# Kernel optimization log

Measured on AMD Instinct MI355X. Metric: run time of the kernel, lower is better.

Reference implementation:

```python
import jax, jax.numpy as jnp
import numpy as np

D_MODEL = 2048
NHEAD = 16
HEAD_DIM = D_MODEL // NHEAD  # 128
B, S = 2, 2048
THETA = 10000.0


def setup_inputs() -> dict:
    key = jax.random.key(0)
    ks = jax.random.split(key, 10)
    sc = 1.0 / np.sqrt(D_MODEL)
    inp = {
        "x": jax.random.normal(ks[0], (B, S, D_MODEL), dtype=jnp.float32),
        "mask": jnp.tril(jnp.ones((1, 1, S, S), dtype=jnp.int32)),
        "Wq": jax.random.normal(ks[1], (D_MODEL, D_MODEL), dtype=jnp.float32) * sc,
        "bq": jax.random.normal(ks[2], (D_MODEL,), dtype=jnp.float32) * 0.01,
        "Wk": jax.random.normal(ks[3], (D_MODEL, D_MODEL), dtype=jnp.float32) * sc,
        "bk": jax.random.normal(ks[4], (D_MODEL,), dtype=jnp.float32) * 0.01,
        "Wv": jax.random.normal(ks[5], (D_MODEL, D_MODEL), dtype=jnp.float32) * sc,
        "bv": jax.random.normal(ks[6], (D_MODEL,), dtype=jnp.float32) * 0.01,
        "Wo": jax.random.normal(ks[7], (D_MODEL, D_MODEL), dtype=jnp.float32) * sc,
        "bo": jax.random.normal(ks[8], (D_MODEL,), dtype=jnp.float32) * 0.01,
    }
    return inp


def _rope(x):
    # x: [B, H, S, D]; rotary applied to first D/2 dims (per the torch module's chunk(2)).
    D = x.shape[-1]
    half = D // 2            # rotary slice size (64)
    quarter = half // 2      # rotate_half split (32)
    seq = x.shape[2]
    inv_freq = 1.0 / (THETA ** (jnp.arange(0, D, 2, dtype=jnp.float32) / D))  # [D/2]
    t = jnp.arange(seq, dtype=jnp.float32)
    freqs = jnp.einsum("i,j->ij", t, inv_freq)  # [S, D/2]
    # emb = cat(freqs, freqs) then sliced to [:half] == freqs[:, :half]
    cos = jnp.cos(freqs)[None, None, :, :half]  # [1,1,S,half]
    sin = jnp.sin(freqs)[None, None, :, :half]
    x_rope, x_pass = x[..., :half], x[..., half:]
    x1, x2 = x_rope[..., :quarter], x_rope[..., quarter:]
    rotated = jnp.concatenate([-x2, x1], axis=-1)
    x_rope = x_rope * cos + rotated * sin
    return jnp.concatenate([x_rope, x_pass], axis=-1)


def reference(x, mask, Wq, bq, Wk, bk, Wv, bv, Wo, bo):
    b, s, _ = x.shape
    def proj(W, bias):
        y = jnp.einsum("bsd,ed->bse", x, W) + bias  # torch Linear: x @ W.T + b
        return y.reshape(b, s, NHEAD, HEAD_DIM).transpose(0, 2, 1, 3)  # [B,H,S,Dh]
    q = _rope(proj(Wq, bq))
    k = _rope(proj(Wk, bk))
    v = proj(Wv, bv)
    scores = jnp.einsum("bhqd,bhkd->bhqk", q, k) / jnp.sqrt(jnp.float32(HEAD_DIM))
    scores = jnp.where(mask == 0, jnp.float32(-1e9), scores)
    a = jax.nn.softmax(scores, axis=-1)
    o = jnp.einsum("bhqk,bhkd->bhqd", a, v)
    o = o.transpose(0, 2, 1, 3).reshape(b, s, D_MODEL)
    return jnp.einsum("bsd,ed->bse", o, Wo) + bo
```

## Files before the change

kernel.cpp:

```cpp
#include <hip/hip_runtime.h>
#include <stdint.h>
#include <math.h>

typedef short short8 __attribute__((ext_vector_type(8)));
typedef float f32x4 __attribute__((ext_vector_type(4)));

#define S_LEN   2048
#define DMODEL  2048
#define NHEADS  16
#define HDIM    128
#define NBATCH  2
#define BHTOT   32
#define MROWS   4096

#define XB_OFF   ((size_t)0)
#define WQ_OFF   ((size_t)16777216)
#define WK_OFF   ((size_t)25165824)
#define WV_OFF   ((size_t)33554432)
#define Q_OFF    ((size_t)41943040)
#define K_OFF    ((size_t)58720256)
#define VT_OFF   ((size_t)75497472)
#define COS_OFF  ((size_t)92274688)
#define SIN_OFF  ((size_t)92798976)
#define WO_OFF   ((size_t)93323264)
#define WS_NEED  (WO_OFF + (size_t)8388608)

__device__ __forceinline__ unsigned short f2bf(float f) {
  unsigned int u = __float_as_uint(f);
  unsigned int r = (u + 0x7FFFu + ((u >> 16) & 1u)) >> 16;
  return (unsigned short)r;
}
__device__ __forceinline__ float bf2f(unsigned short b) {
  return __uint_as_float(((unsigned int)b) << 16);
}

__device__ __forceinline__ void gl_lds16(const unsigned short* g, unsigned short* l) {
  __builtin_amdgcn_global_load_lds(
      (const __attribute__((address_space(1))) unsigned int*)(g),
      (__attribute__((address_space(3))) unsigned int*)(l),
      16, 0, 0);
}

__global__ __launch_bounds__(256) void k_cvt(const float* __restrict__ src,
                                             unsigned short* __restrict__ dst, int n4) {
  int i = blockIdx.x * 256 + threadIdx.x;
  if (i >= n4) return;
  float4 v = ((const float4*)src)[i];
  ushort4 o;
  o.x = f2bf(v.x); o.y = f2bf(v.y); o.z = f2bf(v.z); o.w = f2bf(v.w);
  ((ushort4*)dst)[i] = o;
}

__global__ __launch_bounds__(256) void k_prep(
    const float* __restrict__ x, const float* __restrict__ Wq,
    const float* __restrict__ Wk, const float* __restrict__ Wv,
    const float* __restrict__ Wo,
    unsigned short* __restrict__ xb, unsigned short* __restrict__ wqb,
    unsigned short* __restrict__ wkb, unsigned short* __restrict__ wvb,
    unsigned short* __restrict__ wob,
    float* __restrict__ ct, float* __restrict__ st) {
  int i = blockIdx.x * 256 + threadIdx.x;
  if (i < 6291456) {
    const float* s; unsigned short* d; int off;
    if (i < 2097152) { s = x; d = xb; off = i; }
    else {
      int j = i - 2097152, sel = j >> 20;
      off = j & 1048575;
      if (sel == 3) {
        if (!wob) return;
        s = Wo; d = wob;
      } else {
        s = (sel == 0) ? Wq : (sel == 1 ? Wk : Wv);
        d = (sel == 0) ? wqb : (sel == 1 ? wkb : wvb);
      }
    }
    float4 v = ((const float4*)s)[off];
    ushort4 o;
    o.x = f2bf(v.x); o.y = f2bf(v.y); o.z = f2bf(v.z); o.w = f2bf(v.w);
    ((ushort4*)d)[off] = o;
  } else {
    int j = i - 6291456;
    if (j < S_LEN * 64) {
      int s = j >> 6, jj = j & 63;
      float inv = expf(-(float)(2 * jj) * (9.210340371976184f / 128.0f));
      float ang = (float)s * inv;
      ct[j] = cosf(ang);
      st[j] = sinf(ang);
    }
  }
}

#define CP 136
__global__ __launch_bounds__(256) void k_gemm_qkv(
    const unsigned short* __restrict__ xb,
    const unsigned short* __restrict__ wqb, const unsigned short* __restrict__ wkb,
    const unsigned short* __restrict__ wvb,
    const float* __restrict__ bq, const float* __restrict__ bk, const float* __restrict__ bv,
    const float* __restrict__ ct, const float* __restrict__ st,
    unsigned short* __restrict__ qr, unsigned short* __restrict__ kr,
    unsigned short* __restrict__ vt) {
  __shared__ unsigned short SMEM[128 * CP];
  unsigned short* As = SMEM;
  unsigned short* Bs = SMEM + 8192;
  int m0 = blockIdx.x * 128;
  int n0g = blockIdx.y * 128;
  int wsel = n0g >> 11;
  int nw0 = n0g & (DMODEL - 1);
  const unsigned short* W = (wsel == 0) ? wqb : (wsel == 1 ? wkb : wvb);
  const float* bias = (wsel == 0) ? bq : (wsel == 1 ? bk : bv);
  int tid = threadIdx.x, lane = tid & 63, wid = tid >> 6;
  int wr = wid >> 1, wc = wid & 1;
  int lq = lane & 15, lk = lane >> 4;
  int gr = wid * 32 + (lane >> 3);
  int gc = ((lane & 7) * 8) ^ ((lane >> 3) << 3);

  f32x4 acc[4][4];
#pragma unroll
  for (int m = 0; m < 4; m++)
#pragma unroll
    for (int n = 0; n < 4; n++) { acc[m][n][0]=0.f; acc[m][n][1]=0.f; acc[m][n][2]=0.f; acc[m][n][3]=0.f; }

  for (int k0 = 0; k0 < DMODEL; k0 += 64) {
#pragma unroll
    for (int i = 0; i < 4; i++) {
      gl_lds16(xb + (size_t)(m0 + gr + i * 8) * DMODEL + k0 + gc, As + (wid * 32 + i * 8) * 64);
      gl_lds16(W  + (size_t)(nw0 + gr + i * 8) * DMODEL + k0 + gc, Bs + (wid * 32 + i * 8) * 64);
    }
    __syncthreads();
#pragma unroll
    for (int kk = 0; kk < 2; kk++) {
      short8 af[4], bfr[4];
      int sw = (lq & 7) << 3;
#pragma unroll
      for (int m = 0; m < 4; m++)
        af[m] = *(const short8*)&As[(wr * 64 + m * 16 + lq) * 64 + ((kk * 32 + lk * 8) ^ sw)];
#pragma unroll
      for (int n = 0; n < 4; n++)
        bfr[n] = *(const short8*)&Bs[(wc * 64 + n * 16 + lq) * 64 + ((kk * 32 + lk * 8) ^ sw)];
#pragma unroll
      for (int m = 0; m < 4; m++)
#pragma unroll
        for (int n = 0; n < 4; n++)
          acc[m][n] = __builtin_amdgcn_mfma_f32_16x16x32_bf16(af[m], bfr[n], acc[m][n], 0, 0, 0);
    }
    __syncthreads();
  }

  int h = nw0 >> 7, b = m0 >> 11, s0 = m0 & (S_LEN - 1);
  float bi[4];
#pragma unroll
  for (int n = 0; n < 4; n++) bi[n] = bias[nw0 + wc * 64 + n * 16 + lq];

  if (wsel < 2) {
    float qs = (wsel == 0) ? 0.08838834764831843f : 1.0f;
    if (wc == 0) {
#pragma unroll
      for (int m = 0; m < 4; m++) {
        int sl = wr * 64 + m * 16 + lk * 4;
#pragma unroll
        for (int r = 0; r < 4; r++) {
          int s = (s0 + sl + r);
          const float* cb = ct + s * 64;
          const float* sb = st + s * 64;
#pragma unroll
          for (int n = 0; n < 2; n++) {
            int fq = n * 16 + lq;
            float x1 = acc[m][n][r] + bi[n];
            float x2 = acc[m][n + 2][r] + bi[n + 2];
            SMEM[(sl + r) * CP + fq]      = f2bf((x1 * cb[fq]      - x2 * sb[fq])      * qs);
            SMEM[(sl + r) * CP + fq + 32] = f2bf((x2 * cb[fq + 32] + x1 * sb[fq + 32]) * qs);
          }
        }
      }
    } else {
#pragma unroll
      for (int m = 0; m < 4; m++) {
        int sl = wr * 64 + m * 16 + lk * 4;
#pragma unroll
        for (int n = 0; n < 4; n++) {
          int fq = 64 + n * 16 + lq;
#pragma unroll
          for (int r = 0; r < 4; r++)
            SMEM[(sl + r) * CP + fq] = f2bf((acc[m][n][r] + bi[n]) * qs);
        }
      }
    }
    __syncthreads();
    int row = tid >> 1, hf2 = tid & 1;
    unsigned short* dstb = (wsel == 0 ? qr : kr) +
        ((size_t)(b * NHEADS + h) * S_LEN + s0 + row) * HDIM + hf2 * 64;
    const unsigned short* srcb = &SMEM[row * CP + hf2 * 64];
#pragma unroll
    for (int j = 0; j < 8; j++)
      *(short8*)(dstb + j * 8) = *(const short8*)(srcb + j * 8);
  } else {
#pragma unroll
    for (int m = 0; m < 4; m++) {
      int sl = wr * 64 + m * 16 + lk * 4;
#pragma unroll
      for (int n = 0; n < 4; n++) {
        int fq = wc * 64 + n * 16 + lq;
#pragma unroll
        for (int r = 0; r < 4; r++)
          SMEM[fq * CP + sl + r] = f2bf(acc[m][n][r] + bi[n]);
      }
    }
    __syncthreads();
    int row = tid >> 1, hf2 = tid & 1;
    unsigned short* dstb = vt +
        ((size_t)(b * NHEADS + h) * HDIM + row) * S_LEN + s0 + hf2 * 64;
    const unsigned short* srcb = &SMEM[row * CP + hf2 * 64];
#pragma unroll
    for (int j = 0; j < 8; j++)
      *(short8*)(dstb + j * 8) = *(const short8*)(srcb + j * 8);
  }
}

__device__ __forceinline__ void attn_sm_pv(
    f32x4* sacc, f32x4* acco, float* rm, float* rs,
    unsigned short (*Psw)[72], const unsigned short* V0,
    int lq, int lk, int rsw) {
  float mx4[4];
  int need = 0;
#pragma unroll
  for (int r = 0; r < 4; r++) {
    float mx = fmaxf(fmaxf(sacc[0][r], sacc[1][r]), fmaxf(sacc[2][r], sacc[3][r]));
    mx = fmaxf(mx, __shfl_xor(mx, 1, 64));
    mx = fmaxf(mx, __shfl_xor(mx, 2, 64));
    mx = fmaxf(mx, __shfl_xor(mx, 4, 64));
    mx = fmaxf(mx, __shfl_xor(mx, 8, 64));
    mx4[r] = mx;
    need |= (mx - rm[r] > 8.0f) ? 1 : 0;
  }
  if (__any(need)) {
#pragma unroll
    for (int r = 0; r < 4; r++) {
      float mnew = fmaxf(rm[r], mx4[r]);
      float corr = __expf(rm[r] - mnew);
      rs[r] *= corr;
#pragma unroll
      for (int nd = 0; nd < 8; nd++) acco[nd][r] *= corr;
      rm[r] = mnew;
    }
  }
#pragma unroll
  for (int r = 0; r < 4; r++) {
    float psum = 0.f;
#pragma unroll
    for (int n = 0; n < 4; n++) {
      float p = __expf(sacc[n][r] - rm[r]);
      sacc[n][r] = p;
      psum += p;
    }
    rs[r] += psum;
  }
#pragma unroll
  for (int n = 0; n < 4; n++)
#pragma unroll
    for (int r = 0; r < 4; r++)
      Psw[lk * 4 + r][n * 16 + lq] = f2bf(sacc[n][r]);
#pragma unroll
  for (int ks2 = 0; ks2 < 2; ks2++) {
    short8 pa = *(const short8*)&Psw[lq][ks2 * 32 + lk * 8];
#pragma unroll
    for (int nd = 0; nd < 8; nd++) {
      short8 vf = *(const short8*)&V0[(nd * 16 + lq) * 64 + ((ks2 * 32 + lk * 8) ^ rsw)];
      acco[nd] = __builtin_amdgcn_mfma_f32_16x16x32_bf16(pa, vf, acco[nd], 0, 0, 0);
    }
  }
}

__global__ __launch_bounds__(256, 2) void k_attn(
    const unsigned short* __restrict__ qr, const unsigned short* __restrict__ kr,
    const unsigned short* __restrict__ vt, unsigned short* __restrict__ ob) {
  __shared__ unsigned short Kl[2][64 * 128];
  __shared__ unsigned short Vl[2][128 * 64];
  __shared__ unsigned short Ps[4][16][72];
  int bh = blockIdx.x;
  int yy = blockIdx.y;
  int f = (yy < 8) ? yy : 23 - yy;
  int qtA = 31 - f, qtB = f;
  int q0A = qtA * 64, q0B = qtB * 64;
  int b = bh >> 4, h = bh & 15;
  int tid = threadIdx.x, lane = tid & 63, w = tid >> 6;
  int lq = lane & 15, lk = lane >> 4;
  const unsigned short* kbh = kr + (size_t)bh * S_LEN * HDIM;
  const unsigned short* vbh = vt + (size_t)bh * HDIM * S_LEN;
  int ksrow = tid >> 4;
  int kscol = ((tid & 15) * 8) ^ ((ksrow & 7) << 3);
  int vsrow = tid >> 3;
  int vscol = ((tid & 7) * 8) ^ ((vsrow & 7) << 3);
  int ldso = tid * 8;
  int rsw = (lq & 7) << 3;

  const unsigned short* qbA =
      qr + ((size_t)bh * S_LEN + q0A + w * 16 + lq) * HDIM + lk * 8;
  const unsigned short* qbB =
      qr + ((size_t)bh * S_LEN + q0B + w * 16 + lq) * HDIM + lk * 8;
  short8 qfA[4], qfB[4];
#pragma unroll
  for (int ks = 0; ks < 4; ks++) {
    qfA[ks] = *(const short8*)(qbA + ks * 32);
    qfB[ks] = *(const short8*)(qbB + ks * 32);
  }

  f32x4 accoA[8], accoB[8];
#pragma unroll
  for (int nd = 0; nd < 8; nd++) {
    accoA[nd][0]=0.f; accoA[nd][1]=0.f; accoA[nd][2]=0.f; accoA[nd][3]=0.f;
    accoB[nd][0]=0.f; accoB[nd][1]=0.f; accoB[nd][2]=0.f; accoB[nd][3]=0.f;
  }
  float rmA[4], rsA[4], rmB[4], rsB[4];
#pragma unroll
  for (int r = 0; r < 4; r++) { rmA[r] = -3.0e38f; rsA[r] = 0.f; rmB[r] = -3.0e38f; rsB[r] = 0.f; }

#pragma unroll
  for (int c = 0; c < 4; c++) {
    gl_lds16(kbh + (size_t)(c * 16 + ksrow) * HDIM + kscol, &Kl[0][c * 2048 + ldso]);
    gl_lds16(vbh + (size_t)(c * 32 + vsrow) * S_LEN + vscol, &Vl[0][c * 2048 + ldso]);
  }
  __syncthreads();
  int cur = 0;

  for (int t = 0; t <= qtA; t++) {
    int kv0 = t * 64;
    if (t < qtA) {
      int nx = kv0 + 64;
#pragma unroll
      for (int c = 0; c < 4; c++) {
        gl_lds16(kbh + (size_t)(nx + c * 16 + ksrow) * HDIM + kscol,
                 &Kl[cur ^ 1][c * 2048 + ldso]);
        gl_lds16(vbh + (size_t)(c * 32 + vsrow) * S_LEN + nx + vscol,
                 &Vl[cur ^ 1][c * 2048 + ldso]);
      }
    }
    const unsigned short* K0 = &Kl[cur][0];
    const unsigned short* V0 = &Vl[cur][0];
    bool actB = (t <= qtB);

    f32x4 saccA[4], saccB[4];
#pragma unroll
    for (int n = 0; n < 4; n++) {
      saccA[n][0]=0.f; saccA[n][1]=0.f; saccA[n][2]=0.f; saccA[n][3]=0.f;
      saccB[n][0]=0.f; saccB[n][1]=0.f; saccB[n][2]=0.f; saccB[n][3]=0.f;
    }
    if (actB) {
#pragma unroll
      for (int ks = 0; ks < 4; ks++)
#pragma unroll
        for (int n = 0; n < 4; n++) {
          short8 kf = *(const short8*)&K0[(n * 16 + lq) * 128 + ((ks * 32 + lk * 8) ^ rsw)];
          saccA[n] = __builtin_amdgcn_mfma_f32_16x16x32_bf16(qfA[ks], kf, saccA[n], 0, 0, 0);
          saccB[n] = __builtin_amdgcn_mfma_f32_16x16x32_bf16(qfB[ks], kf, saccB[n], 0, 0, 0);
        }
    } else {
#pragma unroll
      for (int ks = 0; ks < 4; ks++)
#pragma unroll
        for (int n = 0; n < 4; n++) {
          short8 kf = *(const short8*)&K0[(n * 16 + lq) * 128 + ((ks * 32 + lk * 8) ^ rsw)];
          saccA[n] = __builtin_amdgcn_mfma_f32_16x16x32_bf16(qfA[ks], kf, saccA[n], 0, 0, 0);
        }
    }
    if (t == qtA) {
#pragma unroll
      for (int n = 0; n < 4; n++)
#pragma unroll
        for (int r = 0; r < 4; r++) {
          int qrow = q0A + w * 16 + lk * 4 + r;
          int kvc = kv0 + n * 16 + lq;
          if (kvc > qrow) saccA[n][r] = -3.0e38f;
        }
    }
    attn_sm_pv(saccA, accoA, rmA, rsA, Ps[w], V0, lq, lk, rsw);
    if (actB) {
      if (t == qtB) {
#pragma unroll
        for (int n = 0; n < 4; n++)
#pragma unroll
          for (int r = 0; r < 4; r++) {
            int qrow = q0B + w * 16 + lk * 4 + r;
            int kvc = kv0 + n * 16 + lq;
            if (kvc > qrow) saccB[n][r] = -3.0e38f;
          }
      }
      attn_sm_pv(saccB, accoB, rmB, rsB, Ps[w], V0, lq, lk, rsw);
    }
    __syncthreads();
    cur ^= 1;
  }

#pragma unroll
  for (int r = 0; r < 4; r++) {
    float sA = rsA[r];
    sA += __shfl_xor(sA, 1, 64);
    sA += __shfl_xor(sA, 2, 64);
    sA += __shfl_xor(sA, 4, 64);
    sA += __shfl_xor(sA, 8, 64);
    float invA = 1.0f / sA;
    int srowA = q0A + w * 16 + lk * 4 + r;
    unsigned short* dstA = ob + ((size_t)b * S_LEN + srowA) * DMODEL + h * HDIM;
#pragma unroll
    for (int nd = 0; nd < 8; nd++) dstA[nd * 16 + lq] = f2bf(accoA[nd][r] * invA);
    float sB = rsB[r];
    sB += __shfl_xor(sB, 1, 64);
    sB += __shfl_xor(sB, 2, 64);
    sB += __shfl_xor(sB, 4, 64);
    sB += __shfl_xor(sB, 8, 64);
    float invB = 1.0f / sB;
    int srowB = q0B + w * 16 + lk * 4 + r;
    unsigned short* dstB = ob + ((size_t)b * S_LEN + srowB) * DMODEL + h * HDIM;
#pragma unroll
    for (int nd = 0; nd < 8; nd++) dstB[nd * 16 + lq] = f2bf(accoB[nd][r] * invB);
  }
}

__global__ __launch_bounds__(256) void k_gemm_out(
    const unsigned short* __restrict__ ob, const unsigned short* __restrict__ wob,
    const float* __restrict__ bo, float* __restrict__ out) {
  __shared__ unsigned short As[128][64];
  __shared__ unsigned short Bs[128][64];
  int m0 = blockIdx.x * 128, n0 = blockIdx.y * 128;
  int tid = threadIdx.x, lane = tid & 63, wid = tid >> 6;
  int wr = wid >> 1, wc = wid & 1;
  int lq = lane & 15, lk = lane >> 4;
  int gr = wid * 32 + (lane >> 3);
  int gc = ((lane & 7) * 8) ^ ((lane >> 3) << 3);

  f32x4 acc[4][4];
#pragma unroll
  for (int m = 0; m < 4; m++)
#pragma unroll
    for (int n = 0; n < 4; n++) { acc[m][n][0]=0.f; acc[m][n][1]=0.f; acc[m][n][2]=0.f; acc[m][n][3]=0.f; }

  for (int k0 = 0; k0 < DMODEL; k0 += 64) {
#pragma unroll
    for (int i = 0; i < 4; i++) {
      gl_lds16(ob  + (size_t)(m0 + gr + i * 8) * DMODEL + k0 + gc, &As[wid * 32 + i * 8][0]);
      gl_lds16(wob + (size_t)(n0 + gr + i * 8) * DMODEL + k0 + gc, &Bs[wid * 32 + i * 8][0]);
    }
    __syncthreads();
#pragma unroll
    for (int kk = 0; kk < 2; kk++) {
      short8 af[4], bfr[4];
      int sw = (lq & 7) << 3;
#pragma unroll
      for (int m = 0; m < 4; m++)
        af[m] = *(const short8*)&As[wr * 64 + m * 16 + lq][(kk * 32 + lk * 8) ^ sw];
#pragma unroll
      for (int n = 0; n < 4; n++)
        bfr[n] = *(const short8*)&Bs[wc * 64 + n * 16 + lq][(kk * 32 + lk * 8) ^ sw];
#pragma unroll
      for (int m = 0; m < 4; m++)
#pragma unroll
        for (int n = 0; n < 4; n++)
          acc[m][n] = __builtin_amdgcn_mfma_f32_16x16x32_bf16(af[m], bfr[n], acc[m][n], 0, 0, 0);
    }
    __syncthreads();
  }
#pragma unroll
  for (int n = 0; n < 4; n++) {
    int el = n0 + wc * 64 + n * 16 + lq;
    float bi = bo[el];
#pragma unroll
    for (int m = 0; m < 4; m++) {
      int row = m0 + wr * 64 + m * 16 + lk * 4;
#pragma unroll
      for (int r = 0; r < 4; r++)
        out[(size_t)(row + r) * DMODEL + el] = acc[m][n][r] + bi;
    }
  }
}

extern "C" void kernel_launch(void* const* d_in, const int* in_sizes, int n_in,
                              void* d_out, int out_size, void* d_ws, size_t ws_size,
                              hipStream_t stream) {
  const float* x  = (const float*)d_in[0];
  const float* Wq = (const float*)d_in[2];
  const float* bq = (const float*)d_in[3];
  const float* Wk = (const float*)d_in[4];
  const float* bk = (const float*)d_in[5];
  const float* Wv = (const float*)d_in[6];
  const float* bv = (const float*)d_in[7];
  const float* Wo = (const float*)d_in[8];
  const float* bo = (const float*)d_in[9];
  float* out = (float*)d_out;
  char* ws = (char*)d_ws;

  unsigned short* xb  = (unsigned short*)(ws + XB_OFF);
  unsigned short* wqb = (unsigned short*)(ws + WQ_OFF);
  unsigned short* wkb = (unsigned short*)(ws + WK_OFF);
  unsigned short* wvb = (unsigned short*)(ws + WV_OFF);
  unsigned short* qr  = (unsigned short*)(ws + Q_OFF);
  unsigned short* kr  = (unsigned short*)(ws + K_OFF);
  unsigned short* vt  = (unsigned short*)(ws + VT_OFF);
  float* ct = (float*)(ws + COS_OFF);
  float* st = (float*)(ws + SIN_OFF);
  bool haveWo = (ws_size >= WS_NEED);
  unsigned short* wob = haveWo ? (unsigned short*)(ws + WO_OFF) : nullptr;

  k_prep<<<25088, 256, 0, stream>>>(x, Wq, Wk, Wv, Wo, xb, wqb, wkb, wvb, wob, ct, st);
  k_gemm_qkv<<<dim3(MROWS / 128, 6144 / 128), 256, 0, stream>>>(
      xb, wqb, wkb, wvb, bq, bk, bv, ct, st, qr, kr, vt);
  if (!haveWo)
    k_cvt<<<(DMODEL * DMODEL / 4 + 255) / 256, 256, 0, stream>>>(Wo, wqb, DMODEL * DMODEL / 4);
  k_attn<<<dim3(BHTOT, 16), 256, 0, stream>>>(qr, kr, vt, xb);
  k_gemm_out<<<dim3(MROWS / 128, DMODEL / 128), 256, 0, stream>>>(
      xb, haveWo ? wob : wqb, bo, out);
}
```

Measured before the change: 259.3 us.

## Double-buffer LDS tiles in QKV and output projection GEMMs

Both projection GEMM kernels now keep two LDS stages and issue the global-to-LDS loads for the next K tile before the MFMA work on the current tile. The aim is to overlap global memory latency with matrix compute and drop one barrier per iteration. In exchange, LDS per block doubles to 64 KB, which may lower occupancy. The epilogue of the QKV kernel may have reused SMEM with the CP-padded layout, and the allocation changed from 128*CP to 32768 elements, so that reuse needs to stay within bounds.

Result: faster. 232.0 us, median of 2 (-10.5%).

```diff
diff --git a/kernel.cpp b/kernel.cpp
--- a/kernel.cpp
+++ b/kernel.cpp
@@ -99,9 +99,7 @@
     const float* __restrict__ ct, const float* __restrict__ st,
     unsigned short* __restrict__ qr, unsigned short* __restrict__ kr,
     unsigned short* __restrict__ vt) {
-  __shared__ unsigned short SMEM[128 * CP];
-  unsigned short* As = SMEM;
-  unsigned short* Bs = SMEM + 8192;
+  __shared__ unsigned short SMEM[32768];
   int m0 = blockIdx.x * 128;
   int n0g = blockIdx.y * 128;
   int wsel = n0g >> 11;
@@ -113,6 +111,7 @@
   int lq = lane & 15, lk = lane >> 4;
   int gr = wid * 32 + (lane >> 3);
   int gc = ((lane & 7) * 8) ^ ((lane >> 3) << 3);
+  int lbase = (wid * 32) * 64;
 
   f32x4 acc[4][4];
 #pragma unroll
@@ -120,23 +119,36 @@
 #pragma unroll
     for (int n = 0; n < 4; n++) { acc[m][n][0]=0.f; acc[m][n][1]=0.f; acc[m][n][2]=0.f; acc[m][n][3]=0.f; }
 
+#pragma unroll
+  for (int i = 0; i < 4; i++) {
+    gl_lds16(xb + (size_t)(m0 + gr + i * 8) * DMODEL + gc, SMEM + lbase + i * 512);
+    gl_lds16(W  + (size_t)(nw0 + gr + i * 8) * DMODEL + gc, SMEM + 8192 + lbase + i * 512);
+  }
+  __syncthreads();
+  int cur = 0;
+
   for (int k0 = 0; k0 < DMODEL; k0 += 64) {
-#pragma unroll
-    for (int i = 0; i < 4; i++) {
-      gl_lds16(xb + (size_t)(m0 + gr + i * 8) * DMODEL + k0 + gc, As + (wid * 32 + i * 8) * 64);
-      gl_lds16(W  + (size_t)(nw0 + gr + i * 8) * DMODEL + k0 + gc, Bs + (wid * 32 + i * 8) * 64);
-    }
-    __syncthreads();
+    if (k0 + 64 < DMODEL) {
+      int kn = k0 + 64;
+      unsigned short* An = SMEM + (cur ^ 1) * 16384;
+#pragma unroll
+      for (int i = 0; i < 4; i++) {
+        gl_lds16(xb + (size_t)(m0 + gr + i * 8) * DMODEL + kn + gc, An + lbase + i * 512);
+        gl_lds16(W  + (size_t)(nw0 + gr + i * 8) * DMODEL + kn + gc, An + 8192 + lbase + i * 512);
+      }
+    }
+    const unsigned short* Ac = SMEM + cur * 16384;
+    const unsigned short* Bc = Ac + 8192;
 #pragma unroll
     for (int kk = 0; kk < 2; kk++) {
       short8 af[4], bfr[4];
       int sw = (lq & 7) << 3;
 #pragma unroll
       for (int m = 0; m < 4; m++)
-        af[m] = *(const short8*)&As[(wr * 64 + m * 16 + lq) * 64 + ((kk * 32 + lk * 8) ^ sw)];
+        af[m] = *(const short8*)&Ac[(wr * 64 + m * 16 + lq) * 64 + ((kk * 32 + lk * 8) ^ sw)];
 #pragma unroll
       for (int n = 0; n < 4; n++)
-        bfr[n] = *(const short8*)&Bs[(wc * 64 + n * 16 + lq) * 64 + ((kk * 32 + lk * 8) ^ sw)];
+        bfr[n] = *(const short8*)&Bc[(wc * 64 + n * 16 + lq) * 64 + ((kk * 32 + lk * 8) ^ sw)];
 #pragma unroll
       for (int m = 0; m < 4; m++)
 #pragma unroll
@@ -144,6 +156,7 @@
           acc[m][n] = __builtin_amdgcn_mfma_f32_16x16x32_bf16(af[m], bfr[n], acc[m][n], 0, 0, 0);
     }
     __syncthreads();
+    cur ^= 1;
   }
 
   int h = nw0 >> 7, b = m0 >> 11, s0 = m0 & (S_LEN - 1);
@@ -418,14 +431,14 @@
 __global__ __launch_bounds__(256) void k_gemm_out(
     const unsigned short* __restrict__ ob, const unsigned short* __restrict__ wob,
     const float* __restrict__ bo, float* __restrict__ out) {
-  __shared__ unsigned short As[128][64];
-  __shared__ unsigned short Bs[128][64];
+  __shared__ unsigned short SMEM[32768];
   int m0 = blockIdx.x * 128, n0 = blockIdx.y * 128;
   int tid = threadIdx.x, lane = tid & 63, wid = tid >> 6;
   int wr = wid >> 1, wc = wid & 1;
   int lq = lane & 15, lk = lane >> 4;
   int gr = wid * 32 + (lane >> 3);
   int gc = ((lane & 7) * 8) ^ ((lane >> 3) << 3);
+  int lbase = (wid * 32) * 64;
 
   f32x4 acc[4][4];
 #pragma unroll
@@ -433,23 +446,36 @@
 #pragma unroll
     for (int n = 0; n < 4; n++) { acc[m][n][0]=0.f; acc[m][n][1]=0.f; acc[m][n][2]=0.f; acc[m][n][3]=0.f; }
 
+#pragma unroll
+  for (int i = 0; i < 4; i++) {
+    gl_lds16(ob  + (size_t)(m0 + gr + i * 8) * DMODEL + gc, SMEM + lbase + i * 512);
+    gl_lds16(wob + (size_t)(n0 + gr + i * 8) * DMODEL + gc, SMEM + 8192 + lbase + i * 512);
+  }
+  __syncthreads();
+  int cur = 0;
+
   for (int k0 = 0; k0 < DMODEL; k0 += 64) {
-#pragma unroll
-    for (int i = 0; i < 4; i++) {
-      gl_lds16(ob  + (size_t)(m0 + gr + i * 8) * DMODEL + k0 + gc, &As[wid * 32 + i * 8][0]);
-      gl_lds16(wob + (size_t)(n0 + gr + i * 8) * DMODEL + k0 + gc, &Bs[wid * 32 + i * 8][0]);
-    }
-    __syncthreads();
+    if (k0 + 64 < DMODEL) {
+      int kn = k0 + 64;
+      unsigned short* An = SMEM + (cur ^ 1) * 16384;
+#pragma unroll
+      for (int i = 0; i < 4; i++) {
+        gl_lds16(ob  + (size_t)(m0 + gr + i * 8) * DMODEL + kn + gc, An + lbase + i * 512);
+        gl_lds16(wob + (size_t)(n0 + gr + i * 8) * DMODEL + kn + gc, An + 8192 + lbase + i * 512);
+      }
+    }
+    const unsigned short* Ac = SMEM + cur * 16384;
+    const unsigned short* Bc = Ac + 8192;
 #pragma unroll
     for (int kk = 0; kk < 2; kk++) {
       short8 af[4], bfr[4];
       int sw = (lq & 7) << 3;
 #pragma unroll
       for (int m = 0; m < 4; m++)
-        af[m] = *(const short8*)&As[wr * 64 + m * 16 + lq][(kk * 32 + lk * 8) ^ sw];
+        af[m] = *(const short8*)&Ac[(wr * 64 + m * 16 + lq) * 64 + ((kk * 32 + lk * 8) ^ sw)];
 #pragma unroll
       for (int n = 0; n < 4; n++)
-        bfr[n] = *(const short8*)&Bs[wc * 64 + n * 16 + lq][(kk * 32 + lk * 8) ^ sw];
+        bfr[n] = *(const short8*)&Bc[(wc * 64 + n * 16 + lq) * 64 + ((kk * 32 + lk * 8) ^ sw)];
 #pragma unroll
       for (int m = 0; m < 4; m++)
 #pragma unroll
@@ -457,6 +483,7 @@
           acc[m][n] = __builtin_amdgcn_mfma_f32_16x16x32_bf16(af[m], bfr[n], acc[m][n], 0, 0, 0);
     }
     __syncthreads();
+    cur ^= 1;
   }
 #pragma unroll
   for (int n = 0; n < 4; n++) {
```

## Double-buffer B tile in LDS and load A fragments directly into registers

Applied to the files above, without the earlier changes.

Both the QKV and output GEMMs are rewritten around a shared macro body. The B (weight) tile is double-buffered in LDS, with the next tile prefetched while the current one is computed. The A operand is loaded from global memory straight into registers, ping-ponging between two register sets, instead of being staged through LDS. This aims to overlap global loads with MFMA work and halve LDS traffic, at the cost of more VGPRs, uncoalesced direct A loads, and possible occupancy loss.

After: 503.3 us. +94.1%, slower.

```diff
diff --git a/kernel.cpp b/kernel.cpp
--- a/kernel.cpp
+++ b/kernel.cpp
@@ -90,6 +90,106 @@
   }
 }
 
+#define LOAD_A(S, kn)                                  \
+    S##0 = *(const short8*)(arow0 + (kn));             \
+    S##1 = *(const short8*)(arow1 + (kn));             \
+    S##2 = *(const short8*)(arow2 + (kn));             \
+    S##3 = *(const short8*)(arow3 + (kn));             \
+    S##4 = *(const short8*)(arow0 + (kn) + 32);        \
+    S##5 = *(const short8*)(arow1 + (kn) + 32);        \
+    S##6 = *(const short8*)(arow2 + (kn) + 32);        \
+    S##7 = *(const short8*)(arow3 + (kn) + 32);
+
+#define STAGE_B(BP, kn, dst)                                                            \
+    gl_lds16((BP) + (size_t)(nb0 + gr     ) * DMODEL + (kn) + gc, (dst) + (wid*32     )*64); \
+    gl_lds16((BP) + (size_t)(nb0 + gr +  8) * DMODEL + (kn) + gc, (dst) + (wid*32 +  8)*64); \
+    gl_lds16((BP) + (size_t)(nb0 + gr + 16) * DMODEL + (kn) + gc, (dst) + (wid*32 + 16)*64); \
+    gl_lds16((BP) + (size_t)(nb0 + gr + 24) * DMODEL + (kn) + gc, (dst) + (wid*32 + 24)*64);
+
+#define COMPUTE_STEP(S)                                                                  \
+    { const unsigned short* Bc = SMEM + cur * 8192;                                      \
+      short8 b0, b1, b2, b3;                                                             \
+      b0 = *(const short8*)&Bc[(wc*64 +  0 + lq)*64 + ((lk*8) ^ sw)];                    \
+      b1 = *(const short8*)&Bc[(wc*64 + 16 + lq)*64 + ((lk*8) ^ sw)];                    \
+      b2 = *(const short8*)&Bc[(wc*64 + 32 + lq)*64 + ((lk*8) ^ sw)];                    \
+      b3 = *(const short8*)&Bc[(wc*64 + 48 + lq)*64 + ((lk*8) ^ sw)];                    \
+      acc[0][0] = __builtin_amdgcn_mfma_f32_16x16x32_bf16(S##0, b0, acc[0][0], 0,0,0);   \
+      acc[1][0] = __builtin_amdgcn_mfma_f32_16x16x32_bf16(S##1, b0, acc[1][0], 0,0,0);   \
+      acc[2][0] = __builtin_amdgcn_mfma_f32_16x16x32_bf16(S##2, b0, acc[2][0], 0,0,0);   \
+      acc[3][0] = __builtin_amdgcn_mfma_f32_16x16x32_bf16(S##3, b0, acc[3][0], 0,0,0);   \
+      acc[0][1] = __builtin_amdgcn_mfma_f32_16x16x32_bf16(S##0, b1, acc[0][1], 0,0,0);   \
+      acc[1][1] = __builtin_amdgcn_mfma_f32_16x16x32_bf16(S##1, b1, acc[1][1], 0,0,0);   \
+      acc[2][1] = __builtin_amdgcn_mfma_f32_16x16x32_bf16(S##2, b1, acc[2][1], 0,0,0);   \
+      acc[3][1] = __builtin_amdgcn_mfma_f32_16x16x32_bf16(S##3, b1, acc[3][1], 0,0,0);   \
+      acc[0][2] = __builtin_amdgcn_mfma_f32_16x16x32_bf16(S##0, b2, acc[0][2], 0,0,0);   \
+      acc[1][2] = __builtin_amdgcn_mfma_f32_16x16x32_bf16(S##1, b2, acc[1][2], 0,0,0);   \
+      acc[2][2] = __builtin_amdgcn_mfma_f32_16x16x32_bf16(S##2, b2, acc[2][2], 0,0,0);   \
+      acc[3][2] = __builtin_amdgcn_mfma_f32_16x16x32_bf16(S##3, b2, acc[3][2], 0,0,0);   \
+      acc[0][3] = __builtin_amdgcn_mfma_f32_16x16x32_bf16(S##0, b3, acc[0][3], 0,0,0);   \
+      acc[1][3] = __builtin_amdgcn_mfma_f32_16x16x32_bf16(S##1, b3, acc[1][3], 0,0,0);   \
+      acc[2][3] = __builtin_amdgcn_mfma_f32_16x16x32_bf16(S##2, b3, acc[2][3], 0,0,0);   \
+      acc[3][3] = __builtin_amdgcn_mfma_f32_16x16x32_bf16(S##3, b3, acc[3][3], 0,0,0);   \
+      b0 = *(const short8*)&Bc[(wc*64 +  0 + lq)*64 + ((32 + lk*8) ^ sw)];               \
+      b1 = *(const short8*)&Bc[(wc*64 + 16 + lq)*64 + ((32 + lk*8) ^ sw)];               \
+      b2 = *(const short8*)&Bc[(wc*64 + 32 + lq)*64 + ((32 + lk*8) ^ sw)];               \
+      b3 = *(const short8*)&Bc[(wc*64 + 48 + lq)*64 + ((32 + lk*8) ^ sw)];               \
+      acc[0][0] = __builtin_amdgcn_mfma_f32_16x16x32_bf16(S##4, b0, acc[0][0], 0,0,0);   \
+      acc[1][0] = __builtin_amdgcn_mfma_f32_16x16x32_bf16(S##5, b0, acc[1][0], 0,0,0);   \
+      acc[2][0] = __builtin_amdgcn_mfma_f32_16x16x32_bf16(S##6, b0, acc[2][0], 0,0,0);   \
+      acc[3][0] = __builtin_amdgcn_mfma_f32_16x16x32_bf16(S##7, b0, acc[3][0], 0,0,0);   \
+      acc[0][1] = __builtin_amdgcn_mfma_f32_16x16x32_bf16(S##4, b1, acc[0][1], 0,0,0);   \
+      acc[1][1] = __builtin_amdgcn_mfma_f32_16x16x32_bf16(S##5, b1, acc[1][1], 0,0,0);   \
+      acc[2][1] = __builtin_amdgcn_mfma_f32_16x16x32_bf16(S##6, b1, acc[2][1], 0,0,0);   \
+      acc[3][1] = __builtin_amdgcn_mfma_f32_16x16x32_bf16(S##7, b1, acc[3][1], 0,0,0);   \
+      acc[0][2] = __builtin_amdgcn_mfma_f32_16x16x32_bf16(S##4, b2, acc[0][2], 0,0,0);   \
+      acc[1][2] = __builtin_amdgcn_mfma_f32_16x16x32_bf16(S##5, b2, acc[1][2], 0,0,0);   \
+      acc[2][2] = __builtin_amdgcn_mfma_f32_16x16x32_bf16(S##6, b2, acc[2][2], 0,0,0);   \
+      acc[3][2] = __builtin_amdgcn_mfma_f32_16x16x32_bf16(S##7, b2, acc[3][2], 0,0,0);   \
+      acc[0][3] = __builtin_amdgcn_mfma_f32_16x16x32_bf16(S##4, b3, acc[0][3], 0,0,0);   \
+      acc[1][3] = __builtin_amdgcn_mfma_f32_16x16x32_bf16(S##5, b3, acc[1][3], 0,0,0);   \
+      acc[2][3] = __builtin_amdgcn_mfma_f32_16x16x32_bf16(S##6, b3, acc[2][3], 0,0,0);   \
+      acc[3][3] = __builtin_amdgcn_mfma_f32_16x16x32_bf16(S##7, b3, acc[3][3], 0,0,0); }
+
+#define GEMM_PRE_BODY(APTR, BPTR)                                                 \
+  int tid = threadIdx.x, lane = tid & 63, wid = tid >> 6;                         \
+  int wr = wid >> 1, wc = wid & 1;                                                \
+  int lq = lane & 15, lk = lane >> 4;                                             \
+  int gr = wid * 32 + (lane >> 3);                                                \
+  int gc = ((lane & 7) * 8) ^ ((lane >> 3) << 3);                                 \
+  int sw = (lq & 7) << 3;                                                         \
+  const unsigned short* arow0 = (APTR) + (size_t)(m0 + wr*64 +  0 + lq) * DMODEL + lk*8; \
+  const unsigned short* arow1 = (APTR) + (size_t)(m0 + wr*64 + 16 + lq) * DMODEL + lk*8; \
+  const unsigned short* arow2 = (APTR) + (size_t)(m0 + wr*64 + 32 + lq) * DMODEL + lk*8; \
+  const unsigned short* arow3 = (APTR) + (size_t)(m0 + wr*64 + 48 + lq) * DMODEL + lk*8; \
+  f32x4 acc[4][4];                                                                \
+  _Pragma("unroll")                                                               \
+  for (int m = 0; m < 4; m++)                                                     \
+    _Pragma("unroll")                                                             \
+    for (int n = 0; n < 4; n++) { acc[m][n][0]=0.f; acc[m][n][1]=0.f; acc[m][n][2]=0.f; acc[m][n][3]=0.f; } \
+  short8 Aa0,Aa1,Aa2,Aa3,Aa4,Aa5,Aa6,Aa7;                                         \
+  short8 Ab0,Ab1,Ab2,Ab3,Ab4,Ab5,Ab6,Ab7;                                         \
+                              \
+  STAGE_B(BPTR, 0, SMEM)                                                          \
+  LOAD_A(Aa, 0)                                                                   \
+  __syncthreads();                                                                \
+  int cur = 0;                                                                    \
+  for (int k0 = 0; k0 < DMODEL; k0 += 128) {                                      \
+    if (k0 + 64 < DMODEL) {                                                       \
+      unsigned short* Bn = SMEM + (cur ^ 1) * 8192;                               \
+      STAGE_B(BPTR, k0 + 64, Bn)                                                  \
+      LOAD_A(Ab, k0 + 64)                                                         \
+    }                                                                             \
+    COMPUTE_STEP(Aa)                                                              \
+    __syncthreads(); cur ^= 1;                                                    \
+    if (k0 + 128 < DMODEL) {                                                      \
+      unsigned short* Bn = SMEM + (cur ^ 1) * 8192;                               \
+      STAGE_B(BPTR, k0 + 128, Bn)                                                 \
+      LOAD_A(Aa, k0 + 128)                                                        \
+    }                                                                             \
+    COMPUTE_STEP(Ab)                                                              \
+    __syncthreads(); cur ^= 1;                                                    \
+  }
+
 #define CP 136
 __global__ __launch_bounds__(256) void k_gemm_qkv(
     const unsigned short* __restrict__ xb,
@@ -99,57 +199,20 @@
     const float* __restrict__ ct, const float* __restrict__ st,
     unsigned short* __restrict__ qr, unsigned short* __restrict__ kr,
     unsigned short* __restrict__ vt) {
-  __shared__ unsigned short SMEM[128 * CP];
-  unsigned short* As = SMEM;
-  unsigned short* Bs = SMEM + 8192;
+  __shared__ unsigned short SMEM[17408];
   int m0 = blockIdx.x * 128;
   int n0g = blockIdx.y * 128;
   int wsel = n0g >> 11;
-  int nw0 = n0g & (DMODEL - 1);
+  int nb0 = n0g & (DMODEL - 1);
   const unsigned short* W = (wsel == 0) ? wqb : (wsel == 1 ? wkb : wvb);
   const float* bias = (wsel == 0) ? bq : (wsel == 1 ? bk : bv);
-  int tid = threadIdx.x, lane = tid & 63, wid = tid >> 6;
-  int wr = wid >> 1, wc = wid & 1;
-  int lq = lane & 15, lk = lane >> 4;
-  int gr = wid * 32 + (lane >> 3);
-  int gc = ((lane & 7) * 8) ^ ((lane >> 3) << 3);
-
-  f32x4 acc[4][4];
-#pragma unroll
-  for (int m = 0; m < 4; m++)
-#pragma unroll
-    for (int n = 0; n < 4; n++) { acc[m][n][0]=0.f; acc[m][n][1]=0.f; acc[m][n][2]=0.f; acc[m][n][3]=0.f; }
-
-  for (int k0 = 0; k0 < DMODEL; k0 += 64) {
-#pragma unroll
-    for (int i = 0; i < 4; i++) {
-      gl_lds16(xb + (size_t)(m0 + gr + i * 8) * DMODEL + k0 + gc, As + (wid * 32 + i * 8) * 64);
-      gl_lds16(W  + (size_t)(nw0 + gr + i * 8) * DMODEL + k0 + gc, Bs + (wid * 32 + i * 8) * 64);
-    }
-    __syncthreads();
-#pragma unroll
-    for (int kk = 0; kk < 2; kk++) {
-      short8 af[4], bfr[4];
-      int sw = (lq & 7) << 3;
-#pragma unroll
-      for (int m = 0; m < 4; m++)
-        af[m] = *(const short8*)&As[(wr * 64 + m * 16 + lq) * 64 + ((kk * 32 + lk * 8) ^ sw)];
-#pragma unroll
-      for (int n = 0; n < 4; n++)
-        bfr[n] = *(const short8*)&Bs[(wc * 64 + n * 16 + lq) * 64 + ((kk * 32 + lk * 8) ^ sw)];
-#pragma unroll
-      for (int m = 0; m < 4; m++)
-#pragma unroll
-        for (int n = 0; n < 4; n++)
-          acc[m][n] = __builtin_amdgcn_mfma_f32_16x16x32_bf16(af[m], bfr[n], acc[m][n], 0, 0, 0);
-    }
-    __syncthreads();
-  }
-
-  int h = nw0 >> 7, b = m0 >> 11, s0 = m0 & (S_LEN - 1);
+
+  GEMM_PRE_BODY(xb, W)
+
+  int h = nb0 >> 7, b = m0 >> 11, s0 = m0 & (S_LEN - 1);
   float bi[4];
 #pragma unroll
-  for (int n = 0; n < 4; n++) bi[n] = bias[nw0 + wc * 64 + n * 16 + lq];
+  for (int n = 0; n < 4; n++) bi[n] = bias[nb0 + wc * 64 + n * 16 + lq];
 
   if (wsel < 2) {
     float qs = (wsel == 0) ? 0.08838834764831843f : 1.0f;
@@ -213,6 +276,29 @@
 #pragma unroll
     for (int j = 0; j < 8; j++)
       *(short8*)(dstb + j * 8) = *(const short8*)(srcb + j * 8);
+  }
+}
+
+__global__ __launch_bounds__(256) void k_gemm_out(
+    const unsigned short* __restrict__ ob, const unsigned short* __restrict__ wob,
+    const float* __restrict__ bo, float* __restrict__ out) {
+  __shared__ unsigned short SMEM[16384];
+  int m0 = blockIdx.x * 128;
+  int nb0 = blockIdx.y * 128;
+
+  GEMM_PRE_BODY(ob, wob)
+
+#pragma unroll
+  for (int n = 0; n < 4; n++) {
+    int el = nb0 + wc * 64 + n * 16 + lq;
+    float bi = bo[el];
+#pragma unroll
+    for (int m = 0; m < 4; m++) {
+      int row = m0 + wr * 64 + m * 16 + lk * 4;
+#pragma unroll
+      for (int r = 0; r < 4; r++)
+        out[(size_t)(row + r) * DMODEL + el] = acc[m][n][r] + bi;
+    }
   }
 }
 
@@ -415,63 +501,6 @@
   }
 }
 
-__global__ __launch_bounds__(256) void k_gemm_out(
-    const unsigned short* __restrict__ ob, const unsigned short* __restrict__ wob,
-    const float* __restrict__ bo, float* __restrict__ out) {
-  __shared__ unsigned short As[128][64];
-  __shared__ unsigned short Bs[128][64];
-  int m0 = blockIdx.x * 128, n0 = blockIdx.y * 128;
-  int tid = threadIdx.x, lane = tid & 63, wid = tid >> 6;
-  int wr = wid >> 1, wc = wid & 1;
-  int lq = lane & 15, lk = lane >> 4;
-  int gr = wid * 32 + (lane >> 3);
-  int gc = ((lane & 7) * 8) ^ ((lane >> 3) << 3);
-
-  f32x4 acc[4][4];
-#pragma unroll
-  for (int m = 0; m < 4; m++)
-#pragma unroll
-    for (int n = 0; n < 4; n++) { acc[m][n][0]=0.f; acc[m][n][1]=0.f; acc[m][n][2]=0.f; acc[m][n][3]=0.f; }
-
-  for (int k0 = 0; k0 < DMODEL; k0 += 64) {
-#pragma unroll
-    for (int i = 0; i < 4; i++) {
-      gl_lds16(ob  + (size_t)(m0 + gr + i * 8) * DMODEL + k0 + gc, &As[wid * 32 + i * 8][0]);
-      gl_lds16(wob + (size_t)(n0 + gr + i * 8) * DMODEL + k0 + gc, &Bs[wid * 32 + i * 8][0]);
-    }
-    __syncthreads();
-#pragma unroll
-    for (int kk = 0; kk < 2; kk++) {
-      short8 af[4], bfr[4];
-      int sw = (lq & 7) << 3;
-#pragma unroll
-      for (int m = 0; m < 4; m++)
-        af[m] = *(const short8*)&As[wr * 64 + m * 16 + lq][(kk * 32 + lk * 8) ^ sw];
-#pragma unroll
-      for (int n = 0; n < 4; n++)
-        bfr[n] = *(const short8*)&Bs[wc * 64 + n * 16 + lq][(kk * 32 + lk * 8) ^ sw];
-#pragma unroll
-      for (int m = 0; m < 4; m++)
-#pragma unroll
-        for (int n = 0; n < 4; n++)
-          acc[m][n] = __builtin_amdgcn_mfma_f32_16x16x32_bf16(af[m], bfr[n], acc[m][n], 0, 0, 0);
-    }
-    __syncthreads();
-  }
-#pragma unroll
-  for (int n = 0; n < 4; n++) {
-    int el = n0 + wc * 64 + n * 16 + lq;
-    float bi = bo[el];
-#pragma unroll
-    for (int m = 0; m < 4; m++) {
-      int row = m0 + wr * 64 + m * 16 + lk * 4;
-#pragma unroll
-      for (int r = 0; r < 4; r++)
-        out[(size_t)(row + r) * DMODEL + el] = acc[m][n][r] + bi;
-    }
-  }
-}
-
 extern "C" void kernel_launch(void* const* d_in, const int* in_sizes, int n_in,
                               void* d_out, int out_size, void* d_ws, size_t ws_size,
                               hipStream_t stream) {
```
